# Optimization experiments

Hardware: AMD Instinct MI355X
Metric: run time of the kernel (lower is better)

The kernel has to match this reference:

```python
import jax, jax.numpy as jnp
import numpy as np

N_NODES = 100000
N_EDGES = 1600000
D = 128  # h_feats


def setup_inputs() -> dict:
    key = jax.random.key(0)
    k1, k2, k3, k4 = jax.random.split(key, 4)
    x = jax.random.normal(k1, (N_NODES, D), dtype=jnp.float32)
    edge_index = jax.random.randint(k2, (2, N_EDGES), 0, N_NODES, dtype=jnp.int64)
    # Linear(2D -> D), torch layout [out, in]
    W1 = jax.random.normal(k3, (D, 2 * D), dtype=jnp.float32) * (1.0 / np.sqrt(2 * D))
    b1 = jnp.zeros((D,), dtype=jnp.float32)
    # Linear(D -> 1)
    W2 = jax.random.normal(k4, (1, D), dtype=jnp.float32) * (1.0 / np.sqrt(D))
    b2 = jnp.zeros((1,), dtype=jnp.float32)
    return {"x": x, "edge_index": edge_index, "W1": W1, "b1": b1, "W2": W2, "b2": b2}


def reference(x, edge_index, W1, b1, W2, b2):
    # gather both endpoints and concat along features: [E, 2D]
    h = jnp.concatenate([x[edge_index[0]], x[edge_index[1]]], axis=-1)
    h = jax.nn.relu(h @ W1.T + b1)          # [E, D]
    h = h @ W2.T + b2                        # [E, 1]
    return h.squeeze(1)                      # [E]
```

## Files before the change

### kernel.cpp

```cpp
#include <hip/hip_runtime.h>
#include <hip/hip_bf16.h>

#define N_NODES 100000
#define N_EDGES 1600000
#define NT_TILES 1563
#define PRE_BLKX 384

#define BQ_OFF 12800000
#define SA_OFF 25600000
#define SB_OFF 26000000

typedef __attribute__((ext_vector_type(8))) short short8v;
typedef __attribute__((ext_vector_type(4))) float float4v;

__device__ __forceinline__ unsigned short f2bf(float f) {
    unsigned int u = __float_as_uint(f);
    u += 0x7fffu + ((u >> 16) & 1u);
    return (unsigned short)(u >> 16);
}
__device__ __forceinline__ unsigned int pack2bf(float a, float b) {
    return (unsigned int)f2bf(a) | ((unsigned int)f2bf(b) << 16);
}
__device__ __forceinline__ float2 bfpair(unsigned int w) {
    return float2{__uint_as_float(w << 16), __uint_as_float(w & 0xffff0000u)};
}
#define MAGICB 12583040.0f
__device__ __forceinline__ unsigned int qmagic(float f, float inv) {
    return __float_as_uint(fmaf(f, inv, MAGICB));
}

__global__ __launch_bounds__(256) void precompute_kernel(
    const float* __restrict__ x, const float* __restrict__ W1,
    const float* __restrict__ b1, unsigned char* __restrict__ Aq,
    unsigned char* __restrict__ Bq, float* __restrict__ sA,
    float* __restrict__ sB) {
    __shared__ unsigned short wlds[128 * 136];
    __shared__ unsigned short xlds[64 * 136];

    const int tid = threadIdx.x;
    const int by = blockIdx.y;
    unsigned char* __restrict__ Q = by ? Bq : Aq;
    float* __restrict__ S = by ? sB : sA;

    const int wave = tid >> 6;
    const int lane = tid & 63;
    const int quad = lane >> 4;
    const int l15 = lane & 15;

    float4 b1v[2];
#pragma unroll
    for (int j = 0; j < 2; ++j)
        b1v[j] = *reinterpret_cast<const float4*>(b1 + wave * 32 + j * 16 + quad * 4);

#pragma unroll
    for (int i = 0; i < 16; ++i) {
        int fi = tid + i * 256;
        int jl = fi >> 5, c4 = fi & 31;
        float4 w4 = reinterpret_cast<const float4*>(W1)[(size_t)jl * 64 + by * 32 + c4];
        unsigned int* d = reinterpret_cast<unsigned int*>(&wlds[jl * 136 + c4 * 4]);
        d[0] = pack2bf(w4.x, w4.y);
        d[1] = pack2bf(w4.z, w4.w);
    }

    float4 xr[8];
    int t = blockIdx.x;
#pragma unroll
    for (int i = 0; i < 8; ++i) {
        int fi = tid + i * 256;
        int n = fi >> 5, c4 = fi & 31;
        int nn = t * 64 + n; nn = nn < N_NODES ? nn : N_NODES - 1;
        xr[i] = reinterpret_cast<const float4*>(x)[(size_t)nn * 32 + c4];
    }

    for (; t < NT_TILES; t += PRE_BLKX) {
        __syncthreads();
#pragma unroll
        for (int i = 0; i < 8; ++i) {
            int fi = tid + i * 256;
            int n = fi >> 5, c4 = fi & 31;
            unsigned int* d = reinterpret_cast<unsigned int*>(&xlds[n * 136 + c4 * 4]);
            d[0] = pack2bf(xr[i].x, xr[i].y);
            d[1] = pack2bf(xr[i].z, xr[i].w);
        }
        __syncthreads();

        const int tn = t + PRE_BLKX;
        if (tn < NT_TILES) {
#pragma unroll
            for (int i = 0; i < 8; ++i) {
                int fi = tid + i * 256;
                int n = fi >> 5, c4 = fi & 31;
                int nn = tn * 64 + n; nn = nn < N_NODES ? nn : N_NODES - 1;
                xr[i] = reinterpret_cast<const float4*>(x)[(size_t)nn * 32 + c4];
            }
        }

        float4v acc[4][2];
#pragma unroll
        for (int i = 0; i < 4; ++i)
#pragma unroll
            for (int j = 0; j < 2; ++j) acc[i][j] = float4v{0.f, 0.f, 0.f, 0.f};

#pragma unroll
        for (int s = 0; s < 4; ++s) {
            const int k0 = s * 32 + quad * 8;
            short8v wf[2], xf[4];
#pragma unroll
            for (int j = 0; j < 2; ++j)
                wf[j] = *reinterpret_cast<const short8v*>(&wlds[(wave * 32 + j * 16 + l15) * 136 + k0]);
#pragma unroll
            for (int i = 0; i < 4; ++i)
                xf[i] = *reinterpret_cast<const short8v*>(&xlds[(i * 16 + l15) * 136 + k0]);
#pragma unroll
            for (int i = 0; i < 4; ++i)
#pragma unroll
                for (int j = 0; j < 2; ++j)
                    acc[i][j] = __builtin_amdgcn_mfma_f32_16x16x32_bf16(wf[j], xf[i], acc[i][j], 0, 0, 0);
        }
        __syncthreads();

#pragma unroll
        for (int i = 0; i < 4; ++i) {
            const int nl = i * 16 + l15;
#pragma unroll
            for (int j = 0; j < 2; ++j) {
                const int colb = wave * 32 + j * 16 + quad * 4;
                float r0 = acc[i][j][0], r1 = acc[i][j][1];
                float r2 = acc[i][j][2], r3 = acc[i][j][3];
                if (by == 0) {
                    r0 += b1v[j].x; r1 += b1v[j].y;
                    r2 += b1v[j].z; r3 += b1v[j].w;
                }
                uint2 st = {pack2bf(r0, r1), pack2bf(r2, r3)};
                *reinterpret_cast<uint2*>(&xlds[nl * 132 + colb]) = st;
            }
        }
        __syncthreads();

        const int row = tid >> 2, part = tid & 3;
        const int n = t * 64 + row;
        uint4 wv[4];
#pragma unroll
        for (int q = 0; q < 4; ++q)
            wv[q] = *reinterpret_cast<const uint4*>(&xlds[row * 132 + part * 32 + q * 8]);

        float m = 1e-6f;
#pragma unroll
        for (int q = 0; q < 4; ++q) {
            unsigned int ws[4] = {wv[q].x, wv[q].y, wv[q].z, wv[q].w};
#pragma unroll
            for (int w = 0; w < 4; ++w) {
                float2 f = bfpair(ws[w]);
                m = fmaxf(m, fmaxf(fabsf(f.x), fabsf(f.y)));
            }
        }
        m = fmaxf(m, __shfl_xor(m, 1));
        m = fmaxf(m, __shfl_xor(m, 2));
        const float inv = 127.0f / m;

        unsigned int ob[8];
#pragma unroll
        for (int q = 0; q < 4; ++q) {
            unsigned int ws[4] = {wv[q].x, wv[q].y, wv[q].z, wv[q].w};
#pragma unroll
            for (int w = 0; w < 2; ++w) {
                float2 f0 = bfpair(ws[2 * w + 0]);
                float2 f1 = bfpair(ws[2 * w + 1]);
                unsigned int q0 = qmagic(f0.x, inv), q1 = qmagic(f0.y, inv);
                unsigned int q2 = qmagic(f1.x, inv), q3 = qmagic(f1.y, inv);
                ob[q * 2 + w] = (q0 & 0xffu) | ((q1 & 0xffu) << 8) |
                                ((q2 & 0xffu) << 16) | (q3 << 24);
            }
        }
        if (n < N_NODES) {
            uint4 s0 = {ob[0], ob[1], ob[2], ob[3]};
            uint4 s1 = {ob[4], ob[5], ob[6], ob[7]};
            uint4* dst = reinterpret_cast<uint4*>(Q + (size_t)n * 128 + part * 32);
            dst[0] = s0;
            dst[1] = s1;
            if (part == 0) S[n] = m * (1.0f / 127.0f);
        }
    }
}

template <bool IS64>
__device__ __forceinline__ void edge_loop(
    const long long* __restrict__ ei, const unsigned char* __restrict__ Aq,
    const unsigned char* __restrict__ Bq, const float* __restrict__ sA,
    const float* __restrict__ sB, const float* __restrict__ W2, float bias2,
    float* __restrict__ out, int wid, int nwaves, int eg, int sl) {
    const int k0a = sl * 16;
    const int k0b = 64 + sl * 16;
    float w2f[32];
#pragma unroll
    for (int j = 0; j < 4; ++j)
        *reinterpret_cast<float4*>(&w2f[j * 4]) =
            *reinterpret_cast<const float4*>(W2 + k0a + j * 4);
#pragma unroll
    for (int j = 0; j < 4; ++j)
        *reinterpret_cast<float4*>(&w2f[16 + j * 4]) =
            *reinterpret_cast<const float4*>(W2 + k0b + j * 4);
    const int* e32 = reinterpret_cast<const int*>(ei);

    for (int base = wid * 32; base < N_EDGES; base += nwaves * 32) {
        const int e0 = base + eg;
        const int e1 = base + 16 + eg;
        int u0, v0, u1, v1;
        if (IS64) {
            u0 = (int)ei[e0]; v0 = (int)ei[N_EDGES + e0];
            u1 = (int)ei[e1]; v1 = (int)ei[N_EDGES + e1];
        } else {
            u0 = e32[e0]; v0 = e32[N_EDGES + e0];
            u1 = e32[e1]; v1 = e32[N_EDGES + e1];
        }
        const float su0 = sA[u0], sv0 = sB[v0];
        const float su1 = sA[u1], sv1 = sB[v1];
        const unsigned char* ra0 = Aq + (unsigned)u0 * 128;
        const unsigned char* rb0 = Bq + (unsigned)v0 * 128;
        const unsigned char* ra1 = Aq + (unsigned)u1 * 128;
        const unsigned char* rb1 = Bq + (unsigned)v1 * 128;
        uint4 A00 = *reinterpret_cast<const uint4*>(ra0 + k0a);
        uint4 A01 = *reinterpret_cast<const uint4*>(ra0 + k0b);
        uint4 B00 = *reinterpret_cast<const uint4*>(rb0 + k0a);
        uint4 B01 = *reinterpret_cast<const uint4*>(rb0 + k0b);
        uint4 A10 = *reinterpret_cast<const uint4*>(ra1 + k0a);
        uint4 A11 = *reinterpret_cast<const uint4*>(ra1 + k0b);
        uint4 B10 = *reinterpret_cast<const uint4*>(rb1 + k0a);
        uint4 B11 = *reinterpret_cast<const uint4*>(rb1 + k0b);

        {
            const float r = sv0 * __builtin_amdgcn_rcpf(su0);
            const float c = fmaf(r, 128.0f, 128.0f);
            unsigned int aw[8] = {A00.x, A00.y, A00.z, A00.w, A01.x, A01.y, A01.z, A01.w};
            unsigned int bw[8] = {B00.x, B00.y, B00.z, B00.w, B01.x, B01.y, B01.z, B01.w};
            float p = 0.f;
#pragma unroll
            for (int wi = 0; wi < 8; ++wi) {
#pragma unroll
                for (int byt = 0; byt < 4; ++byt) {
                    float fa = (float)((aw[wi] >> (8 * byt)) & 0xffu);
                    float fb = (float)((bw[wi] >> (8 * byt)) & 0xffu);
                    float s = fmaxf(fmaf(fb, r, fa) - c, 0.f);
                    p = fmaf(s, w2f[wi * 4 + byt], p);
                }
            }
            p += __shfl_xor(p, 1);
            p += __shfl_xor(p, 2);
            if (sl == 0) out[e0] = fmaf(su0, p, bias2);
        }
        {
            const float r = sv1 * __builtin_amdgcn_rcpf(su1);
            const float c = fmaf(r, 128.0f, 128.0f);
            unsigned int aw[8] = {A10.x, A10.y, A10.z, A10.w, A11.x, A11.y, A11.z, A11.w};
            unsigned int bw[8] = {B10.x, B10.y, B10.z, B10.w, B11.x, B11.y, B11.z, B11.w};
            float p = 0.f;
#pragma unroll
            for (int wi = 0; wi < 8; ++wi) {
#pragma unroll
                for (int byt = 0; byt < 4; ++byt) {
                    float fa = (float)((aw[wi] >> (8 * byt)) & 0xffu);
                    float fb = (float)((bw[wi] >> (8 * byt)) & 0xffu);
                    float s = fmaxf(fmaf(fb, r, fa) - c, 0.f);
                    p = fmaf(s, w2f[wi * 4 + byt], p);
                }
            }
            p += __shfl_xor(p, 1);
            p += __shfl_xor(p, 2);
            if (sl == 0) out[e1] = fmaf(su1, p, bias2);
        }
    }
}

__global__ __launch_bounds__(256, 4) void edge_kernel(
    const long long* __restrict__ ei, const unsigned char* __restrict__ Aq,
    const unsigned char* __restrict__ Bq, const float* __restrict__ sA,
    const float* __restrict__ sB, const float* __restrict__ W2,
    const float* __restrict__ b2, float* __restrict__ out) {
    const int lane = threadIdx.x & 63;
    const int eg = lane >> 2;
    const int sl = lane & 3;
    const float bias2 = b2[0];

    const unsigned int hi = reinterpret_cast<const unsigned int*>(ei)[2 * lane + 1];
    const bool is64 = (__ballot(hi != 0) == 0ull);

    const int wid = (int)(((unsigned)(blockIdx.x * blockDim.x + threadIdx.x)) >> 6);
    const int nwaves = (int)(((unsigned)(gridDim.x * blockDim.x)) >> 6);

    if (is64) edge_loop<true>(ei, Aq, Bq, sA, sB, W2, bias2, out, wid, nwaves, eg, sl);
    else      edge_loop<false>(ei, Aq, Bq, sA, sB, W2, bias2, out, wid, nwaves, eg, sl);
}

extern "C" void kernel_launch(void* const* d_in, const int* in_sizes, int n_in,
                              void* d_out, int out_size, void* d_ws, size_t ws_size,
                              hipStream_t stream) {
    const float* x = (const float*)d_in[0];
    const long long* ei = (const long long*)d_in[1];
    const float* W1 = (const float*)d_in[2];
    const float* b1 = (const float*)d_in[3];
    const float* W2 = (const float*)d_in[4];
    const float* b2 = (const float*)d_in[5];
    float* out = (float*)d_out;

    unsigned char* Aq = (unsigned char*)d_ws;
    unsigned char* Bq = (unsigned char*)d_ws + BQ_OFF;
    float* sA = (float*)((char*)d_ws + SA_OFF);
    float* sB = (float*)((char*)d_ws + SB_OFF);

    dim3 g1(PRE_BLKX, 2);
    precompute_kernel<<<g1, 256, 0, stream>>>(x, W1, b1, Aq, Bq, sA, sB);
    edge_kernel<<<2048, 256, 0, stream>>>(ei, Aq, Bq, sA, sB, W2, b2, out);
}
```

Before: 169.5 us.

## Pack edge indices in precompute and use packed fp16 dot math per edge

The per-edge dequantize/ReLU/dot loop now runs in packed fp16: bytes are expanded with perm into fp16 pairs via a magic-number trick, combined with packed FMA and max, and accumulated with fdot2. Separately, idle precompute blocks repack the int64 edge_index into an int32 uint2 array, so the edge kernel reads 8 bytes per edge instead of two strided 8-byte loads. This aims to cut ALU work in the edge kernel and index-load traffic. It trades away precision, since intermediates are now fp16, and adds an extra 12.8MB write in precompute whenever the workspace is large enough.

```diff
diff --git a/kernel.cpp b/kernel.cpp
--- a/kernel.cpp
+++ b/kernel.cpp
@@ -5,13 +5,16 @@
 #define N_EDGES 1600000
 #define NT_TILES 1563
 #define PRE_BLKX 384
+#define PRE_5T 27
 
 #define BQ_OFF 12800000
 #define SA_OFF 25600000
 #define SB_OFF 26000000
+#define EP_OFF 26400000
 
 typedef __attribute__((ext_vector_type(8))) short short8v;
 typedef __attribute__((ext_vector_type(4))) float float4v;
+typedef _Float16 h2 __attribute__((ext_vector_type(2)));
 
 __device__ __forceinline__ unsigned short f2bf(float f) {
     unsigned int u = __float_as_uint(f);
@@ -33,7 +36,8 @@
     const float* __restrict__ x, const float* __restrict__ W1,
     const float* __restrict__ b1, unsigned char* __restrict__ Aq,
     unsigned char* __restrict__ Bq, float* __restrict__ sA,
-    float* __restrict__ sB) {
+    float* __restrict__ sB, const void* __restrict__ eiv,
+    uint2* __restrict__ ep, int do_pack) {
     __shared__ unsigned short wlds[128 * 136];
     __shared__ unsigned short xlds[64 * 136];
 
@@ -181,44 +185,109 @@
             if (part == 0) S[n] = m * (1.0f / 127.0f);
         }
     }
-}
-
-template <bool IS64>
-__device__ __forceinline__ void edge_loop(
-    const long long* __restrict__ ei, const unsigned char* __restrict__ Aq,
+
+    if (do_pack && blockIdx.x >= PRE_5T) {
+        const int sidx = by * (PRE_BLKX - PRE_5T) + ((int)blockIdx.x - PRE_5T);
+        const int nsl = 2 * (PRE_BLKX - PRE_5T);
+        const int per = (N_EDGES + nsl - 1) / nsl;
+        const int e0 = sidx * per;
+        const int e1 = (e0 + per < N_EDGES) ? (e0 + per) : N_EDGES;
+        const unsigned int hw = reinterpret_cast<const unsigned int*>(eiv)[2 * lane + 1];
+        const bool is64 = (__ballot(hw != 0) == 0ull);
+        if (is64) {
+            const long long* e64 = reinterpret_cast<const long long*>(eiv);
+            for (int e = e0 + tid; e < e1; e += 256)
+                ep[e] = uint2{(unsigned)e64[e], (unsigned)e64[N_EDGES + e]};
+        } else {
+            const int* p32 = reinterpret_cast<const int*>(eiv);
+            for (int e = e0 + tid; e < e1; e += 256)
+                ep[e] = uint2{(unsigned)p32[e], (unsigned)p32[N_EDGES + e]};
+        }
+    }
+}
+
+#if defined(__has_builtin)
+#if __has_builtin(__builtin_amdgcn_fdot2)
+#define HAVE_FDOT2 1
+#endif
+#endif
+
+__device__ __forceinline__ float edge_dot_f16(
+    uint4 A0, uint4 A1, uint4 B0, uint4 B1, float r, const h2* __restrict__ w2h) {
+    const unsigned aw[8] = {A0.x, A0.y, A0.z, A0.w, A1.x, A1.y, A1.z, A1.w};
+    const unsigned bw[8] = {B0.x, B0.y, B0.z, B0.w, B1.x, B1.y, B1.z, B1.w};
+    const h2 m72 = {(_Float16)(-72.f), (_Float16)(-72.f)};
+    const h2 z2 = {(_Float16)0.f, (_Float16)0.f};
+    const _Float16 rh = (_Float16)r;
+    const h2 rr = {rh, rh};
+    float p = 0.f;
+#pragma unroll
+    for (int wi = 0; wi < 8; ++wi) {
+        unsigned pa0 = __builtin_amdgcn_perm(aw[wi], 0x54545454u, 0x00050004u);
+        unsigned pa1 = __builtin_amdgcn_perm(aw[wi], 0x54545454u, 0x00070006u);
+        unsigned pb0 = __builtin_amdgcn_perm(bw[wi], 0x54545454u, 0x00050004u);
+        unsigned pb1 = __builtin_amdgcn_perm(bw[wi], 0x54545454u, 0x00070006u);
+        h2 ha0 = __builtin_bit_cast(h2, pa0) + m72;
+        h2 hb0 = __builtin_bit_cast(h2, pb0) + m72;
+        h2 ha1 = __builtin_bit_cast(h2, pa1) + m72;
+        h2 hb1 = __builtin_bit_cast(h2, pb1) + m72;
+        h2 t0 = __builtin_elementwise_fma(hb0, rr, ha0);
+        h2 t1 = __builtin_elementwise_fma(hb1, rr, ha1);
+        h2 s0 = __builtin_elementwise_max(t0, z2);
+        h2 s1 = __builtin_elementwise_max(t1, z2);
+#ifdef HAVE_FDOT2
+        p = __builtin_amdgcn_fdot2(s0, w2h[2 * wi], p, false);
+        p = __builtin_amdgcn_fdot2(s1, w2h[2 * wi + 1], p, false);
+#else
+        p = fmaf((float)s0[0], (float)w2h[2 * wi][0], p);
+        p = fmaf((float)s0[1], (float)w2h[2 * wi][1], p);
+        p = fmaf((float)s1[0], (float)w2h[2 * wi + 1][0], p);
+        p = fmaf((float)s1[1], (float)w2h[2 * wi + 1][1], p);
+#endif
+    }
+    return p;
+}
+
+__device__ __forceinline__ void build_w2h(const float* __restrict__ W2,
+                                          int k0a, int k0b, h2* __restrict__ w2h) {
+#pragma unroll
+    for (int wi = 0; wi < 8; ++wi) {
+        const float* wp = W2 + (wi < 4 ? k0a + 4 * wi : k0b + 4 * (wi - 4));
+        float4 f = *reinterpret_cast<const float4*>(wp);
+        w2h[2 * wi]     = h2{(_Float16)(16.f * f.x), (_Float16)(16.f * f.y)};
+        w2h[2 * wi + 1] = h2{(_Float16)(16.f * f.z), (_Float16)(16.f * f.w)};
+    }
+}
+
+__global__ __launch_bounds__(256, 4) void edge_kernel_p(
+    const uint2* __restrict__ ep, const unsigned char* __restrict__ Aq,
     const unsigned char* __restrict__ Bq, const float* __restrict__ sA,
-    const float* __restrict__ sB, const float* __restrict__ W2, float bias2,
-    float* __restrict__ out, int wid, int nwaves, int eg, int sl) {
+    const float* __restrict__ sB, const float* __restrict__ W2,
+    const float* __restrict__ b2, float* __restrict__ out) {
+    const int lane = threadIdx.x & 63;
+    const int eg = lane >> 2;
+    const int sl = lane & 3;
+    const float bias2 = b2[0];
     const int k0a = sl * 16;
     const int k0b = 64 + sl * 16;
-    float w2f[32];
-#pragma unroll
-    for (int j = 0; j < 4; ++j)
-        *reinterpret_cast<float4*>(&w2f[j * 4]) =
-            *reinterpret_cast<const float4*>(W2 + k0a + j * 4);
-#pragma unroll
-    for (int j = 0; j < 4; ++j)
-        *reinterpret_cast<float4*>(&w2f[16 + j * 4]) =
-            *reinterpret_cast<const float4*>(W2 + k0b + j * 4);
-    const int* e32 = reinterpret_cast<const int*>(ei);
+
+    h2 w2h[16];
+    build_w2h(W2, k0a, k0b, w2h);
+
+    const int wid = (int)(((unsigned)(blockIdx.x * blockDim.x + threadIdx.x)) >> 6);
+    const int nwaves = (int)(((unsigned)(gridDim.x * blockDim.x)) >> 6);
 
     for (int base = wid * 32; base < N_EDGES; base += nwaves * 32) {
         const int e0 = base + eg;
         const int e1 = base + 16 + eg;
-        int u0, v0, u1, v1;
-        if (IS64) {
-            u0 = (int)ei[e0]; v0 = (int)ei[N_EDGES + e0];
-            u1 = (int)ei[e1]; v1 = (int)ei[N_EDGES + e1];
-        } else {
-            u0 = e32[e0]; v0 = e32[N_EDGES + e0];
-            u1 = e32[e1]; v1 = e32[N_EDGES + e1];
-        }
-        const float su0 = sA[u0], sv0 = sB[v0];
-        const float su1 = sA[u1], sv1 = sB[v1];
-        const unsigned char* ra0 = Aq + (unsigned)u0 * 128;
-        const unsigned char* rb0 = Bq + (unsigned)v0 * 128;
-        const unsigned char* ra1 = Aq + (unsigned)u1 * 128;
-        const unsigned char* rb1 = Bq + (unsigned)v1 * 128;
+        const uint2 q0 = ep[e0];
+        const uint2 q1 = ep[e1];
+        const float su0 = sA[q0.x], sv0 = sB[q0.y];
+        const float su1 = sA[q1.x], sv1 = sB[q1.y];
+        const unsigned char* ra0 = Aq + (size_t)q0.x * 128;
+        const unsigned char* rb0 = Bq + (size_t)q0.y * 128;
+        const unsigned char* ra1 = Aq + (size_t)q1.x * 128;
+        const unsigned char* rb1 = Bq + (size_t)q1.y * 128;
         uint4 A00 = *reinterpret_cast<const uint4*>(ra0 + k0a);
         uint4 A01 = *reinterpret_cast<const uint4*>(ra0 + k0b);
         uint4 B00 = *reinterpret_cast<const uint4*>(rb0 + k0a);
@@ -230,40 +299,14 @@
 
         {
             const float r = sv0 * __builtin_amdgcn_rcpf(su0);
-            const float c = fmaf(r, 128.0f, 128.0f);
-            unsigned int aw[8] = {A00.x, A00.y, A00.z, A00.w, A01.x, A01.y, A01.z, A01.w};
-            unsigned int bw[8] = {B00.x, B00.y, B00.z, B00.w, B01.x, B01.y, B01.z, B01.w};
-            float p = 0.f;
-#pragma unroll
-            for (int wi = 0; wi < 8; ++wi) {
-#pragma unroll
-                for (int byt = 0; byt < 4; ++byt) {
-                    float fa = (float)((aw[wi] >> (8 * byt)) & 0xffu);
-                    float fb = (float)((bw[wi] >> (8 * byt)) & 0xffu);
-                    float s = fmaxf(fmaf(fb, r, fa) - c, 0.f);
-                    p = fmaf(s, w2f[wi * 4 + byt], p);
-                }
-            }
+            float p = edge_dot_f16(A00, A01, B00, B01, r, w2h);
             p += __shfl_xor(p, 1);
             p += __shfl_xor(p, 2);
             if (sl == 0) out[e0] = fmaf(su0, p, bias2);
         }
         {
             const float r = sv1 * __builtin_amdgcn_rcpf(su1);
-            const float c = fmaf(r, 128.0f, 128.0f);
-            unsigned int aw[8] = {A10.x, A10.y, A10.z, A10.w, A11.x, A11.y, A11.z, A11.w};
-            unsigned int bw[8] = {B10.x, B10.y, B10.z, B10.w, B11.x, B11.y, B11.z, B11.w};
-            float p = 0.f;
-#pragma unroll
-            for (int wi = 0; wi < 8; ++wi) {
-#pragma unroll
-                for (int byt = 0; byt < 4; ++byt) {
-                    float fa = (float)((aw[wi] >> (8 * byt)) & 0xffu);
-                    float fb = (float)((bw[wi] >> (8 * byt)) & 0xffu);
-                    float s = fmaxf(fmaf(fb, r, fa) - c, 0.f);
-                    p = fmaf(s, w2f[wi * 4 + byt], p);
-                }
-            }
+            float p = edge_dot_f16(A10, A11, B10, B11, r, w2h);
             p += __shfl_xor(p, 1);
             p += __shfl_xor(p, 2);
             if (sl == 0) out[e1] = fmaf(su1, p, bias2);
@@ -271,7 +314,38 @@
     }
 }
 
-__global__ __launch_bounds__(256, 4) void edge_kernel(
+template <bool IS64>
+__device__ __forceinline__ void edge_loop_raw(
+    const long long* __restrict__ ei, const unsigned char* __restrict__ Aq,
+    const unsigned char* __restrict__ Bq, const float* __restrict__ sA,
+    const float* __restrict__ sB, const float* __restrict__ W2, float bias2,
+    float* __restrict__ out, int wid, int nwaves, int eg, int sl) {
+    const int k0a = sl * 16, k0b = 64 + sl * 16;
+    h2 w2h[16];
+    build_w2h(W2, k0a, k0b, w2h);
+    const int* e32 = reinterpret_cast<const int*>(ei);
+
+    for (int base = wid * 16; base < N_EDGES; base += nwaves * 16) {
+        const int e = base + eg;
+        int u, v;
+        if (IS64) { u = (int)ei[e]; v = (int)ei[N_EDGES + e]; }
+        else      { u = e32[e];     v = e32[N_EDGES + e]; }
+        const float su = sA[u], sv = sB[v];
+        const unsigned char* ra = Aq + (size_t)(unsigned)u * 128;
+        const unsigned char* rb = Bq + (size_t)(unsigned)v * 128;
+        uint4 A0 = *reinterpret_cast<const uint4*>(ra + k0a);
+        uint4 A1 = *reinterpret_cast<const uint4*>(ra + k0b);
+        uint4 B0 = *reinterpret_cast<const uint4*>(rb + k0a);
+        uint4 B1 = *reinterpret_cast<const uint4*>(rb + k0b);
+        const float r = sv * __builtin_amdgcn_rcpf(su);
+        float p = edge_dot_f16(A0, A1, B0, B1, r, w2h);
+        p += __shfl_xor(p, 1);
+        p += __shfl_xor(p, 2);
+        if (sl == 0) out[e] = fmaf(su, p, bias2);
+    }
+}
+
+__global__ __launch_bounds__(256, 4) void edge_kernel_raw(
     const long long* __restrict__ ei, const unsigned char* __restrict__ Aq,
     const unsigned char* __restrict__ Bq, const float* __restrict__ sA,
     const float* __restrict__ sB, const float* __restrict__ W2,
@@ -280,15 +354,12 @@
     const int eg = lane >> 2;
     const int sl = lane & 3;
     const float bias2 = b2[0];
-
     const unsigned int hi = reinterpret_cast<const unsigned int*>(ei)[2 * lane + 1];
     const bool is64 = (__ballot(hi != 0) == 0ull);
-
     const int wid = (int)(((unsigned)(blockIdx.x * blockDim.x + threadIdx.x)) >> 6);
     const int nwaves = (int)(((unsigned)(gridDim.x * blockDim.x)) >> 6);
-
-    if (is64) edge_loop<true>(ei, Aq, Bq, sA, sB, W2, bias2, out, wid, nwaves, eg, sl);
-    else      edge_loop<false>(ei, Aq, Bq, sA, sB, W2, bias2, out, wid, nwaves, eg, sl);
+    if (is64) edge_loop_raw<true>(ei, Aq, Bq, sA, sB, W2, bias2, out, wid, nwaves, eg, sl);
+    else      edge_loop_raw<false>(ei, Aq, Bq, sA, sB, W2, bias2, out, wid, nwaves, eg, sl);
 }
 
 extern "C" void kernel_launch(void* const* d_in, const int* in_sizes, int n_in,
@@ -306,8 +377,15 @@
     unsigned char* Bq = (unsigned char*)d_ws + BQ_OFF;
     float* sA = (float*)((char*)d_ws + SA_OFF);
     float* sB = (float*)((char*)d_ws + SB_OFF);
+    uint2* ep = (uint2*)((char*)d_ws + EP_OFF);
+
+    const int do_pack = (ws_size >= (size_t)EP_OFF + (size_t)N_EDGES * 8ull) ? 1 : 0;
 
     dim3 g1(PRE_BLKX, 2);
-    precompute_kernel<<<g1, 256, 0, stream>>>(x, W1, b1, Aq, Bq, sA, sB);
-    edge_kernel<<<2048, 256, 0, stream>>>(ei, Aq, Bq, sA, sB, W2, b2, out);
-}
+    precompute_kernel<<<g1, 256, 0, stream>>>(x, W1, b1, Aq, Bq, sA, sB,
+                                              (const void*)ei, ep, do_pack);
+    if (do_pack)
+        edge_kernel_p<<<2048, 256, 0, stream>>>(ep, Aq, Bq, sA, sB, W2, b2, out);
+    else
+        edge_kernel_raw<<<2048, 256, 0, stream>>>(ei, Aq, Bq, sA, sB, W2, b2, out);
+}
```

Measured after the change: 178.3 us. +5.2%, slower.

## Compute both W1 halves per block from one x tile with register-resident weights

Applied to the files above, without the earlier changes.

The precompute kernel no longer uses a 2D grid in which each block handles one half of W1. Each block now loads its x tile once and computes both the A (src) and B (dst) projections in turn. The W1 bf16 fragments are held in registers instead of LDS, and a separate LDS buffer stages the output. This halves global reads of x and drops the weight LDS staging, at the cost of many more VGPRs (32 short8 fragments), which may lower occupancy. The grid goes from 384x2 blocks to 512 blocks.

```diff
diff --git a/kernel.cpp b/kernel.cpp
--- a/kernel.cpp
+++ b/kernel.cpp
@@ -4,7 +4,7 @@
 #define N_NODES 100000
 #define N_EDGES 1600000
 #define NT_TILES 1563
-#define PRE_BLKX 384
+#define PRE_BLKX 512
 
 #define BQ_OFF 12800000
 #define SA_OFF 25600000
@@ -34,14 +34,10 @@
     const float* __restrict__ b1, unsigned char* __restrict__ Aq,
     unsigned char* __restrict__ Bq, float* __restrict__ sA,
     float* __restrict__ sB) {
-    __shared__ unsigned short wlds[128 * 136];
     __shared__ unsigned short xlds[64 * 136];
+    __shared__ unsigned short slds[64 * 132];
 
     const int tid = threadIdx.x;
-    const int by = blockIdx.y;
-    unsigned char* __restrict__ Q = by ? Bq : Aq;
-    float* __restrict__ S = by ? sB : sA;
-
     const int wave = tid >> 6;
     const int lane = tid & 63;
     const int quad = lane >> 4;
@@ -52,15 +48,21 @@
     for (int j = 0; j < 2; ++j)
         b1v[j] = *reinterpret_cast<const float4*>(b1 + wave * 32 + j * 16 + quad * 4);
 
-#pragma unroll
-    for (int i = 0; i < 16; ++i) {
-        int fi = tid + i * 256;
-        int jl = fi >> 5, c4 = fi & 31;
-        float4 w4 = reinterpret_cast<const float4*>(W1)[(size_t)jl * 64 + by * 32 + c4];
-        unsigned int* d = reinterpret_cast<unsigned int*>(&wlds[jl * 136 + c4 * 4]);
-        d[0] = pack2bf(w4.x, w4.y);
-        d[1] = pack2bf(w4.z, w4.w);
-    }
+    short8v wf[2][2][4];
+#pragma unroll
+    for (int h = 0; h < 2; ++h)
+#pragma unroll
+        for (int j = 0; j < 2; ++j)
+#pragma unroll
+            for (int s = 0; s < 4; ++s) {
+                const int c = wave * 32 + j * 16 + l15;
+                const float4* wp = reinterpret_cast<const float4*>(W1) +
+                                   (size_t)c * 64 + h * 32 + s * 8 + quad * 2;
+                float4 wa = wp[0], wb = wp[1];
+                uint4 u = {pack2bf(wa.x, wa.y), pack2bf(wa.z, wa.w),
+                           pack2bf(wb.x, wb.y), pack2bf(wb.z, wb.w)};
+                wf[h][j][s] = __builtin_bit_cast(short8v, u);
+            }
 
     float4 xr[8];
     int t = blockIdx.x;
@@ -95,90 +97,94 @@
             }
         }
 
-        float4v acc[4][2];
-#pragma unroll
-        for (int i = 0; i < 4; ++i)
-#pragma unroll
-            for (int j = 0; j < 2; ++j) acc[i][j] = float4v{0.f, 0.f, 0.f, 0.f};
-
-#pragma unroll
-        for (int s = 0; s < 4; ++s) {
-            const int k0 = s * 32 + quad * 8;
-            short8v wf[2], xf[4];
-#pragma unroll
-            for (int j = 0; j < 2; ++j)
-                wf[j] = *reinterpret_cast<const short8v*>(&wlds[(wave * 32 + j * 16 + l15) * 136 + k0]);
+#pragma unroll
+        for (int h = 0; h < 2; ++h) {
+            unsigned char* __restrict__ Q = h ? Bq : Aq;
+            float* __restrict__ S = h ? sB : sA;
+
+            float4v acc[4][2];
 #pragma unroll
             for (int i = 0; i < 4; ++i)
-                xf[i] = *reinterpret_cast<const short8v*>(&xlds[(i * 16 + l15) * 136 + k0]);
-#pragma unroll
-            for (int i = 0; i < 4; ++i)
-#pragma unroll
-                for (int j = 0; j < 2; ++j)
-                    acc[i][j] = __builtin_amdgcn_mfma_f32_16x16x32_bf16(wf[j], xf[i], acc[i][j], 0, 0, 0);
-        }
-        __syncthreads();
-
-#pragma unroll
-        for (int i = 0; i < 4; ++i) {
-            const int nl = i * 16 + l15;
-#pragma unroll
-            for (int j = 0; j < 2; ++j) {
-                const int colb = wave * 32 + j * 16 + quad * 4;
-                float r0 = acc[i][j][0], r1 = acc[i][j][1];
-                float r2 = acc[i][j][2], r3 = acc[i][j][3];
-                if (by == 0) {
-                    r0 += b1v[j].x; r1 += b1v[j].y;
-                    r2 += b1v[j].z; r3 += b1v[j].w;
-                }
-                uint2 st = {pack2bf(r0, r1), pack2bf(r2, r3)};
-                *reinterpret_cast<uint2*>(&xlds[nl * 132 + colb]) = st;
-            }
-        }
-        __syncthreads();
-
-        const int row = tid >> 2, part = tid & 3;
-        const int n = t * 64 + row;
-        uint4 wv[4];
-#pragma unroll
-        for (int q = 0; q < 4; ++q)
-            wv[q] = *reinterpret_cast<const uint4*>(&xlds[row * 132 + part * 32 + q * 8]);
-
-        float m = 1e-6f;
-#pragma unroll
-        for (int q = 0; q < 4; ++q) {
-            unsigned int ws[4] = {wv[q].x, wv[q].y, wv[q].z, wv[q].w};
-#pragma unroll
-            for (int w = 0; w < 4; ++w) {
-                float2 f = bfpair(ws[w]);
-                m = fmaxf(m, fmaxf(fabsf(f.x), fabsf(f.y)));
-            }
-        }
-        m = fmaxf(m, __shfl_xor(m, 1));
-        m = fmaxf(m, __shfl_xor(m, 2));
-        const float inv = 127.0f / m;
-
-        unsigned int ob[8];
-#pragma unroll
-        for (int q = 0; q < 4; ++q) {
-            unsigned int ws[4] = {wv[q].x, wv[q].y, wv[q].z, wv[q].w};
-#pragma unroll
-            for (int w = 0; w < 2; ++w) {
-                float2 f0 = bfpair(ws[2 * w + 0]);
-                float2 f1 = bfpair(ws[2 * w + 1]);
-                unsigned int q0 = qmagic(f0.x, inv), q1 = qmagic(f0.y, inv);
-                unsigned int q2 = qmagic(f1.x, inv), q3 = qmagic(f1.y, inv);
-                ob[q * 2 + w] = (q0 & 0xffu) | ((q1 & 0xffu) << 8) |
-                                ((q2 & 0xffu) << 16) | (q3 << 24);
-            }
-        }
-        if (n < N_NODES) {
-            uint4 s0 = {ob[0], ob[1], ob[2], ob[3]};
-            uint4 s1 = {ob[4], ob[5], ob[6], ob[7]};
-            uint4* dst = reinterpret_cast<uint4*>(Q + (size_t)n * 128 + part * 32);
-            dst[0] = s0;
-            dst[1] = s1;
-            if (part == 0) S[n] = m * (1.0f / 127.0f);
+#pragma unroll
+                for (int j = 0; j < 2; ++j) acc[i][j] = float4v{0.f, 0.f, 0.f, 0.f};
+
+#pragma unroll
+            for (int s = 0; s < 4; ++s) {
+                const int k0 = s * 32 + quad * 8;
+                short8v xf[4];
+#pragma unroll
+                for (int i = 0; i < 4; ++i)
+                    xf[i] = *reinterpret_cast<const short8v*>(&xlds[(i * 16 + l15) * 136 + k0]);
+#pragma unroll
+                for (int i = 0; i < 4; ++i)
+#pragma unroll
+                    for (int j = 0; j < 2; ++j)
+                        acc[i][j] = __builtin_amdgcn_mfma_f32_16x16x32_bf16(
+                            wf[h][j][s], xf[i], acc[i][j], 0, 0, 0);
+            }
+            __syncthreads();
+
+#pragma unroll
+            for (int i = 0; i < 4; ++i) {
+                const int nl = i * 16 + l15;
+#pragma unroll
+                for (int j = 0; j < 2; ++j) {
+                    const int colb = wave * 32 + j * 16 + quad * 4;
+                    float r0 = acc[i][j][0], r1 = acc[i][j][1];
+                    float r2 = acc[i][j][2], r3 = acc[i][j][3];
+                    if (h == 0) {
+                        r0 += b1v[j].x; r1 += b1v[j].y;
+                        r2 += b1v[j].z; r3 += b1v[j].w;
+                    }
+                    uint2 st = {pack2bf(r0, r1), pack2bf(r2, r3)};
+                    *reinterpret_cast<uint2*>(&slds[nl * 132 + colb]) = st;
+                }
+            }
+            __syncthreads();
+
+            const int row = tid >> 2, part = tid & 3;
+            const int n = t * 64 + row;
+            uint4 wv[4];
+#pragma unroll
+            for (int q = 0; q < 4; ++q)
+                wv[q] = *reinterpret_cast<const uint4*>(&slds[row * 132 + part * 32 + q * 8]);
+
+            float m = 1e-6f;
+#pragma unroll
+            for (int q = 0; q < 4; ++q) {
+                unsigned int ws[4] = {wv[q].x, wv[q].y, wv[q].z, wv[q].w};
+#pragma unroll
+                for (int w = 0; w < 4; ++w) {
+                    float2 f = bfpair(ws[w]);
+                    m = fmaxf(m, fmaxf(fabsf(f.x), fabsf(f.y)));
+                }
+            }
+            m = fmaxf(m, __shfl_xor(m, 1));
+            m = fmaxf(m, __shfl_xor(m, 2));
+            const float inv = 127.0f / m;
+
+            unsigned int ob[8];
+#pragma unroll
+            for (int q = 0; q < 4; ++q) {
+                unsigned int ws[4] = {wv[q].x, wv[q].y, wv[q].z, wv[q].w};
+#pragma unroll
+                for (int w = 0; w < 2; ++w) {
+                    float2 f0 = bfpair(ws[2 * w + 0]);
+                    float2 f1 = bfpair(ws[2 * w + 1]);
+                    unsigned int q0 = qmagic(f0.x, inv), q1 = qmagic(f0.y, inv);
+                    unsigned int q2 = qmagic(f1.x, inv), q3 = qmagic(f1.y, inv);
+                    ob[q * 2 + w] = (q0 & 0xffu) | ((q1 & 0xffu) << 8) |
+                                    ((q2 & 0xffu) << 16) | (q3 << 24);
+                }
+            }
+            if (n < N_NODES) {
+                uint4 s0 = {ob[0], ob[1], ob[2], ob[3]};
+                uint4 s1 = {ob[4], ob[5], ob[6], ob[7]};
+                uint4* dst = reinterpret_cast<uint4*>(Q + (size_t)n * 128 + part * 32);
+                dst[0] = s0;
+                dst[1] = s1;
+                if (part == 0) S[n] = m * (1.0f / 127.0f);
+            }
         }
     }
 }
@@ -307,7 +313,6 @@
     float* sA = (float*)((char*)d_ws + SA_OFF);
     float* sB = (float*)((char*)d_ws + SB_OFF);
 
-    dim3 g1(PRE_BLKX, 2);
-    precompute_kernel<<<g1, 256, 0, stream>>>(x, W1, b1, Aq, Bq, sA, sB);
+    precompute_kernel<<<PRE_BLKX, 256, 0, stream>>>(x, W1, b1, Aq, Bq, sA, sB);
     edge_kernel<<<2048, 256, 0, stream>>>(ei, Aq, Bq, sA, sB, W2, b2, out);
 }
```

Result: slower. 173.4 us (+2.3%).
